# Kernel optimization log

Measured on AMD Instinct MI355X. Metric: run time of the kernel, lower is better.

Reference implementation:

```python
import jax, jax.numpy as jnp
import numpy as np

# pywt db4 reconstruction low-pass (rec_lo) coefficients.
_H = np.array([
    0.23037781330885523, 0.7148465705525415, 0.6308807679295904,
    -0.02798376941698385, -0.18703481171888114, 0.030841381835986965,
    0.032883011666982945, -0.010597401784997278], dtype=np.float64)
# pywt dec_lo = _H[::-1]; conv (flipped) correlation kernel = dec_lo[::-1] = _H.
_FLO = _H
# dec_hi[k] = (-1)^(7-k) * _H[k]; correlation kernel = dec_hi[::-1] -> (-1)^k * _H[7-k].
_FHI = np.array([(-1.0) ** k * _H[7 - k] for k in range(8)])
_FILT = jnp.asarray(np.stack([_FLO, _FHI])[:, None, :], dtype=jnp.float32)  # [2,1,8]
_PAD = 7  # filter_len - 1
_LEVEL = 4


def _dwt_step(sig):
    """One pywt dwt level, mode='symmetric'. sig: [N, L] -> (cA, cD), each [N, (L+7)//2]."""
    # symmetric (half-sample) extension by filter_len-1 each side, drop first sample
    # so that stride-2 VALID correlation reproduces pywt's output phase/length.
    xp = jnp.pad(sig, ((0, 0), (_PAD, _PAD)), mode='symmetric')[:, 1:]
    out = jax.lax.conv_general_dilated(
        xp[:, None, :], _FILT, window_strides=(2,), padding='VALID',
        dimension_numbers=('NCH', 'OIH', 'NCH'))  # [N, 2, (L+7)//2]
    return out[:, 0, :], out[:, 1, :]


def setup_inputs() -> dict:
    key = jax.random.key(0)
    x = jax.random.normal(key, (64, 4096, 32), dtype=jnp.float32)  # [B, L, C]
    return {"x": x}


def reference(x):
    """Faithful batched version of pywt.wavedec(x[i,:,j], 'db4', 'symmetric', level=4).
    Returns tuple (cA4, cD4, cD3, cD2, cD1), each [B, C, scale_len]."""
    B, L, C = x.shape
    sig = jnp.transpose(x, (0, 2, 1)).reshape(B * C, L)
    details = []
    for _ in range(_LEVEL):
        sig, cd = _dwt_step(sig)
        details.append(cd)
    coeffs = [sig] + details[::-1]  # [cA_L, cD_L, ..., cD_1] like pywt.wavedec
    return tuple(c.reshape(B, C, c.shape[-1]) for c in coeffs)
```

## Files before the change

### kernel.cpp

```cpp
#include <hip/hip_runtime.h>


#define NCH 8
#define LPX 634
#define LP1 322
#define LP2 166
#define LP3 86

template <int R, bool LAST>
__device__ __forceinline__ void level_run(
    const float* __restrict__ src, int LPS, int srclo,
    float* __restrict__ dst, int LPD, int DL,
    int lo, int hi,
    float* __restrict__ gcd, int ownLo, int ownHi,
    float* __restrict__ gca, int c, int slot) {
    constexpr float FLO[8] = {
        0.23037781330885523f,  0.7148465705525415f,  0.6308807679295904f,
        -0.02798376941698385f, -0.18703481171888114f, 0.030841381835986965f,
        0.032883011666982945f, -0.010597401784997278f};
    constexpr float FHI[8] = {
        -0.010597401784997278f, -0.032883011666982945f, 0.030841381835986965f,
        0.18703481171888114f,  -0.02798376941698385f,  -0.6308807679295904f,
        0.7148465705525415f,   -0.23037781330885523f};

    const int span = hi - lo;
    int i0r = slot * R;
    if (i0r > span - R) i0r = span - R;
    const int i0 = lo + i0r;

    const float2* row2 = reinterpret_cast<const float2*>(src + c * LPS);
    int p = i0 - (srclo >> 1);
    float2 f0 = row2[p], f1 = row2[p + 1], f2 = row2[p + 2];
    float* drow = LAST ? nullptr : dst + c * LPD;

#pragma unroll
    for (int r = 0; r < R; ++r) {
        const float2 f3 = row2[p + 3 + r];
        const int i = i0 + r;
        const float w0 = f0.x, w1 = f0.y, w2 = f1.x, w3 = f1.y;
        const float w4 = f2.x, w5 = f2.y, w6 = f3.x, w7 = f3.y;
        float a = FLO[0] * w0;
        a = fmaf(FLO[1], w1, a); a = fmaf(FLO[2], w2, a); a = fmaf(FLO[3], w3, a);
        a = fmaf(FLO[4], w4, a); a = fmaf(FLO[5], w5, a); a = fmaf(FLO[6], w6, a);
        a = fmaf(FLO[7], w7, a);
        float d = FHI[0] * w0;
        d = fmaf(FHI[1], w1, d); d = fmaf(FHI[2], w2, d); d = fmaf(FHI[3], w3, d);
        d = fmaf(FHI[4], w4, d); d = fmaf(FHI[5], w5, d); d = fmaf(FHI[6], w6, d);
        d = fmaf(FHI[7], w7, d);

        if constexpr (!LAST) {
            drow[i - lo + 6] = a;
            if (lo == 0 && i < 6) drow[5 - i] = a;
            if (hi == DL && i >= DL - 7) drow[(2 * DL - 1 - i) - lo + 6] = a;
        } else {
            gca[i] = a;
        }
        if (i >= ownLo && i < ownHi) gcd[i] = d;
        f0 = f1; f1 = f2; f2 = f3;
    }
}

__global__ __launch_bounds__(256) void fused_dwt_kernel(
    const float* __restrict__ x, float* __restrict__ out) {
    __shared__ __align__(16) float bx[NCH * LPX];
    __shared__ __align__(16) float b1[NCH * LP1];
    __shared__ __align__(16) float b2[NCH * LP2];
    __shared__ __align__(16) float b3[NCH * LP3];

    const int bid = blockIdx.x;
    const int work = (bid & 7) * 256 + (bid >> 3);
    const int cg = work & 3;
    const int tile = (work >> 2) & 7;
    const int b = work >> 5;

    const int tid = threadIdx.x;
    const int c = tid & 7;
    const int slot = tid >> 3;
    const int c0 = cg * 8;

    const int L0 = 4096, L1 = 2051, L2 = 1029, L3 = 518, L4 = 262;

    const int lo4 = tile * 33, hi4 = min(L4, lo4 + 33);
    const int lo3 = max(0, 2 * lo4 - 6), hi3 = min(L3, 2 * hi4);
    const int lo2 = max(0, 2 * lo3 - 6), hi2 = min(L2, 2 * hi3);
    const int lo1 = max(0, 2 * lo2 - 6), hi1 = min(L1, 2 * hi2);
    const int lox = max(0, 2 * lo1 - 6), hix = min(L0, 2 * hi1);

    const float* xb = x + (size_t)b * L0 * 32 + c0;
    const int nx = hix - lox;
    for (int q = tid; q < nx * 2; q += 256) {
        const int jj = q >> 1;
        const int h = (q & 1) * 4;
        const int t = lox + jj;
        const float4 v = *reinterpret_cast<const float4*>(xb + (size_t)t * 32 + h);
        const float vv[4] = {v.x, v.y, v.z, v.w};
#pragma unroll
        for (int hh = 0; hh < 4; ++hh) {
            float* row = bx + (h + hh) * LPX;
            row[jj + 6] = vv[hh];
            if (lox == 0 && t < 6) row[5 - t] = vv[hh];
            if (hix == L0 && t >= L0 - 7) row[(2 * L0 - 1 - t) - lox + 6] = vv[hh];
        }
    }
    __syncthreads();

    const size_t S = 2048;
    const size_t sig = (size_t)b * 32 + c0 + c;
    float* gca4 = out + sig * L4;
    float* gcd4 = out + S * (size_t)L4 + sig * L4;
    float* gcd3 = out + 2 * S * (size_t)L4 + sig * L3;
    float* gcd2 = out + 2 * S * (size_t)L4 + S * (size_t)L3 + sig * L2;
    float* gcd1 = out + 2 * S * (size_t)L4 + S * (size_t)L3 + S * (size_t)L2 + sig * L1;

    const int o1lo = tile ? 264 * tile - 34 : 0;
    const int o1hi = (tile == 7) ? L1 : 264 * tile + 230;
    const int o2lo = tile ? 132 * tile - 10 : 0;
    const int o2hi = (tile == 7) ? L2 : 132 * tile + 122;
    const int o3lo = tile ? 66 * tile - 2 : 0;
    const int o3hi = (tile == 7) ? L3 : 66 * tile + 64;

    level_run<10, false>(bx, LPX, lox, b1, LP1, L1, lo1, hi1, gcd1, o1lo, o1hi, nullptr, c, slot);
    __syncthreads();
    level_run<5, false>(b1, LP1, lo1, b2, LP2, L2, lo2, hi2, gcd2, o2lo, o2hi, nullptr, c, slot);
    __syncthreads();
    level_run<3, false>(b2, LP2, lo2, b3, LP3, L3, lo3, hi3, gcd3, o3lo, o3hi, nullptr, c, slot);
    __syncthreads();
    level_run<2, true>(b3, LP3, lo3, nullptr, 0, L4, lo4, hi4, gcd4, lo4, hi4, gca4, c, slot);
}

extern "C" void kernel_launch(void* const* d_in, const int* in_sizes, int n_in,
                              void* d_out, int out_size, void* d_ws, size_t ws_size,
                              hipStream_t stream) {
    const float* x = (const float*)d_in[0];
    float* out = (float*)d_out;
    fused_dwt_kernel<<<dim3(2048), dim3(256), 0, stream>>>(x, out);
}
```

Before: 34.22 us.

## Stage detail coefficients in LDS and write them out as coalesced rows

Each level's detail outputs, and the final approximation, are first written to shared-memory staging buffers. All 256 threads then copy them to global memory row by row, giving contiguous stores instead of scattered per-channel strided writes. The channel group shrinks from 8 to 4, so the grid doubles to 4096 blocks and each thread handles fewer outputs per level. This adds shared-memory traffic, extra barriers and duplicated halo loads, and only 4 channels of x are read per block, which means 16-byte reads per 128-byte row.

```diff
diff --git a/kernel.cpp b/kernel.cpp
--- a/kernel.cpp
+++ b/kernel.cpp
@@ -1,19 +1,23 @@
 #include <hip/hip_runtime.h>
 
 
-#define NCH 8
+#define NCH 4
 #define LPX 634
 #define LP1 322
 #define LP2 166
 #define LP3 86
+#define CDPA 314
+#define CDPB 154
+#define CAP4 40
 
 template <int R, bool LAST>
 __device__ __forceinline__ void level_run(
-    const float* __restrict__ src, int LPS, int srclo,
-    float* __restrict__ dst, int LPD, int DL,
+    const float* __restrict__ src, int PS, int srclo,
+    float* __restrict__ dst, int PD, int DL,
     int lo, int hi,
-    float* __restrict__ gcd, int ownLo, int ownHi,
-    float* __restrict__ gca, int c, int slot) {
+    float* __restrict__ cdbuf, int CDP,
+    float* __restrict__ cabuf,
+    int c, int slot) {
     constexpr float FLO[8] = {
         0.23037781330885523f,  0.7148465705525415f,  0.6308807679295904f,
         -0.02798376941698385f, -0.18703481171888114f, 0.030841381835986965f,
@@ -28,10 +32,12 @@
     if (i0r > span - R) i0r = span - R;
     const int i0 = lo + i0r;
 
-    const float2* row2 = reinterpret_cast<const float2*>(src + c * LPS);
+    const float2* row2 = reinterpret_cast<const float2*>(src + c * PS);
     int p = i0 - (srclo >> 1);
     float2 f0 = row2[p], f1 = row2[p + 1], f2 = row2[p + 2];
-    float* drow = LAST ? nullptr : dst + c * LPD;
+    float* drow = LAST ? nullptr : dst + c * PD;
+    float* cdrow = cdbuf + c * CDP - lo;
+    float* carow = LAST ? cabuf + c * CAP4 - lo : nullptr;
 
 #pragma unroll
     for (int r = 0; r < R; ++r) {
@@ -53,10 +59,22 @@
             if (lo == 0 && i < 6) drow[5 - i] = a;
             if (hi == DL && i >= DL - 7) drow[(2 * DL - 1 - i) - lo + 6] = a;
         } else {
-            gca[i] = a;
+            carow[i] = a;
         }
-        if (i >= ownLo && i < ownHi) gcd[i] = d;
+        cdrow[i] = d;
         f0 = f1; f1 = f2; f2 = f3;
+    }
+}
+
+__device__ __forceinline__ void dump_rows(
+    const float* __restrict__ buf, int pitch, int bufLo,
+    float* __restrict__ gbase, int rowLen, int ownLo, int ownHi, int tid) {
+    const int span = ownHi - ownLo;
+#pragma unroll
+    for (int c2 = 0; c2 < NCH; ++c2) {
+        float* g = gbase + (size_t)c2 * rowLen + ownLo;
+        const float* s = buf + c2 * pitch + (ownLo - bufLo);
+        for (int i = tid; i < span; i += 256) g[i] = s[i];
     }
 }
 
@@ -66,17 +84,20 @@
     __shared__ __align__(16) float b1[NCH * LP1];
     __shared__ __align__(16) float b2[NCH * LP2];
     __shared__ __align__(16) float b3[NCH * LP3];
+    __shared__ __align__(16) float cdA[NCH * CDPA];
+    __shared__ __align__(16) float cdB[NCH * CDPB];
+    __shared__ __align__(16) float caB[NCH * CAP4];
 
     const int bid = blockIdx.x;
-    const int work = (bid & 7) * 256 + (bid >> 3);
-    const int cg = work & 3;
-    const int tile = (work >> 2) & 7;
-    const int b = work >> 5;
+    const int work = (bid & 7) * 512 + (bid >> 3);
+    const int cg = work & 7;
+    const int tile = (work >> 3) & 7;
+    const int b = work >> 6;
 
     const int tid = threadIdx.x;
-    const int c = tid & 7;
-    const int slot = tid >> 3;
-    const int c0 = cg * 8;
+    const int c = tid & 3;
+    const int slot = tid >> 2;
+    const int c0 = cg * 4;
 
     const int L0 = 4096, L1 = 2051, L2 = 1029, L3 = 518, L4 = 262;
 
@@ -88,16 +109,14 @@
 
     const float* xb = x + (size_t)b * L0 * 32 + c0;
     const int nx = hix - lox;
-    for (int q = tid; q < nx * 2; q += 256) {
-        const int jj = q >> 1;
-        const int h = (q & 1) * 4;
-        const int t = lox + jj;
-        const float4 v = *reinterpret_cast<const float4*>(xb + (size_t)t * 32 + h);
+    for (int q = tid; q < nx; q += 256) {
+        const int t = lox + q;
+        const float4 v = *reinterpret_cast<const float4*>(xb + (size_t)t * 32);
         const float vv[4] = {v.x, v.y, v.z, v.w};
 #pragma unroll
         for (int hh = 0; hh < 4; ++hh) {
-            float* row = bx + (h + hh) * LPX;
-            row[jj + 6] = vv[hh];
+            float* row = bx + hh * LPX;
+            row[q + 6] = vv[hh];
             if (lox == 0 && t < 6) row[5 - t] = vv[hh];
             if (hix == L0 && t >= L0 - 7) row[(2 * L0 - 1 - t) - lox + 6] = vv[hh];
         }
@@ -105,12 +124,12 @@
     __syncthreads();
 
     const size_t S = 2048;
-    const size_t sig = (size_t)b * 32 + c0 + c;
-    float* gca4 = out + sig * L4;
-    float* gcd4 = out + S * (size_t)L4 + sig * L4;
-    float* gcd3 = out + 2 * S * (size_t)L4 + sig * L3;
-    float* gcd2 = out + 2 * S * (size_t)L4 + S * (size_t)L3 + sig * L2;
-    float* gcd1 = out + 2 * S * (size_t)L4 + S * (size_t)L3 + S * (size_t)L2 + sig * L1;
+    const size_t sigB = (size_t)b * 32 + c0;
+    float* gca4 = out + sigB * L4;
+    float* gcd4 = out + S * (size_t)L4 + sigB * L4;
+    float* gcd3 = out + 2 * S * (size_t)L4 + sigB * L3;
+    float* gcd2 = out + 2 * S * (size_t)L4 + S * (size_t)L3 + sigB * L2;
+    float* gcd1 = out + 2 * S * (size_t)L4 + S * (size_t)L3 + S * (size_t)L2 + sigB * L1;
 
     const int o1lo = tile ? 264 * tile - 34 : 0;
     const int o1hi = (tile == 7) ? L1 : 264 * tile + 230;
@@ -119,13 +138,23 @@
     const int o3lo = tile ? 66 * tile - 2 : 0;
     const int o3hi = (tile == 7) ? L3 : 66 * tile + 64;
 
-    level_run<10, false>(bx, LPX, lox, b1, LP1, L1, lo1, hi1, gcd1, o1lo, o1hi, nullptr, c, slot);
+    level_run<5, false>(bx, LPX, lox, b1, LP1, L1, lo1, hi1, cdA, CDPA, nullptr, c, slot);
     __syncthreads();
-    level_run<5, false>(b1, LP1, lo1, b2, LP2, L2, lo2, hi2, gcd2, o2lo, o2hi, nullptr, c, slot);
+
+    dump_rows(cdA, CDPA, lo1, gcd1, L1, o1lo, o1hi, tid);
+    level_run<3, false>(b1, LP1, lo1, b2, LP2, L2, lo2, hi2, cdB, CDPB, nullptr, c, slot);
     __syncthreads();
-    level_run<3, false>(b2, LP2, lo2, b3, LP3, L3, lo3, hi3, gcd3, o3lo, o3hi, nullptr, c, slot);
+
+    dump_rows(cdB, CDPB, lo2, gcd2, L2, o2lo, o2hi, tid);
+    level_run<2, false>(b2, LP2, lo2, b3, LP3, L3, lo3, hi3, cdA, CDPA, nullptr, c, slot);
     __syncthreads();
-    level_run<2, true>(b3, LP3, lo3, nullptr, 0, L4, lo4, hi4, gcd4, lo4, hi4, gca4, c, slot);
+
+    dump_rows(cdA, CDPA, lo3, gcd3, L3, o3lo, o3hi, tid);
+    level_run<1, true>(b3, LP3, lo3, nullptr, 0, L4, lo4, hi4, cdB, CDPB, caB, c, slot);
+    __syncthreads();
+
+    dump_rows(cdB, CDPB, lo4, gcd4, L4, lo4, hi4, tid);
+    dump_rows(caB, CAP4, lo4, gca4, L4, lo4, hi4, tid);
 }
 
 extern "C" void kernel_launch(void* const* d_in, const int* in_sizes, int n_in,
@@ -133,5 +162,5 @@
                               hipStream_t stream) {
     const float* x = (const float*)d_in[0];
     float* out = (float*)d_out;
-    fused_dwt_kernel<<<dim3(2048), dim3(256), 0, stream>>>(x, out);
+    fused_dwt_kernel<<<dim3(4096), dim3(256), 0, stream>>>(x, out);
 }
```

After: 31.29 us. 1.09x faster.
